# Optimization experiments

Hardware: AMD Instinct MI355X
Metric: run time of the kernel (lower is better)

## Reference

```python
import jax, jax.numpy as jnp
import numpy as np

B, S, D, H, P, K = 2, 1025, 1024, 16, 1024, 32
HD = D // H
G = int(np.sqrt(P))
TEMP = 0.1
CANTOR_W = 0.3
SCALE = HD ** -0.5
EPS_LN = 1e-5


def _layernorm(x, w, b):
    m = jnp.mean(x, axis=-1, keepdims=True)
    v = jnp.mean((x - m) ** 2, axis=-1, keepdims=True)
    return (x - m) * jax.lax.rsqrt(v + EPS_LN) * w + b


def _l2norm(x):
    n = jnp.sqrt(jnp.sum(x * x, axis=-1, keepdims=True))
    return x / jnp.maximum(n, 1e-12)


def _cantor_bias():
    idx = np.arange(P)
    xg, yg = idx % G, idx // G
    s = xg + yg
    z = (s * (s + 1) // 2 + yg).astype(np.float32)
    fp = z / max(z.max(), 1.0)
    dist = np.abs(fp[None, :] - fp[:, None])
    aff = 1.0 - dist
    np.fill_diagonal(aff, -1e9)
    return jnp.asarray(aff * CANTOR_W, dtype=jnp.float32)


def setup_inputs() -> dict:
    key = jax.random.key(0)
    ks = jax.random.split(key, 16)
    std = 0.02
    def w(k, *shape):
        return jax.random.normal(k, shape, dtype=jnp.float32) * std
    inp = {
        'x': jax.random.normal(ks[0], (B, S, D), dtype=jnp.float32),
        'norm1_w': jnp.ones((D,), jnp.float32), 'norm1_b': jnp.zeros((D,), jnp.float32),
        'rq_w': w(ks[1], D, D), 'rq_b': jnp.zeros((D,), jnp.float32),
        'rk_w': w(ks[2], D, D), 'rk_b': jnp.zeros((D,), jnp.float32),
        'pos_bias': _cantor_bias(),
        'qkv_w': w(ks[3], 3 * D, D), 'qkv_b': jnp.zeros((3 * D,), jnp.float32),
        'proj_w': w(ks[4], D, D), 'proj_b': jnp.zeros((D,), jnp.float32),
        'norm2_w': jnp.ones((D,), jnp.float32), 'norm2_b': jnp.zeros((D,), jnp.float32),
        'fc1_w': w(ks[5], 4 * D, D), 'fc1_b': jnp.zeros((4 * D,), jnp.float32),
        'fc2_w': w(ks[6], D, 4 * D), 'fc2_b': jnp.zeros((D,), jnp.float32),
    }
    return inp


def reference(x, norm1_w, norm1_b, rq_w, rq_b, rk_w, rk_b, pos_bias,
              qkv_w, qkv_b, proj_w, proj_b, norm2_w, norm2_b,
              fc1_w, fc1_b, fc2_w, fc2_b):
    x_norm = _layernorm(x, norm1_w, norm1_b)
    # ---- router: content-based top-k wormhole routes over patches ----
    xp = x_norm[:, 1:, :]                                   # [B,P,D]
    q_r = _l2norm(xp @ rq_w.T + rq_b)
    k_r = _l2norm(xp @ rk_w.T + rk_b)
    scores = jnp.einsum('bpd,bqd->bpq', q_r, k_r) + pos_bias[None]
    eye = jnp.eye(P, dtype=bool)
    scores = jnp.where(eye[None], -1e9, scores)
    topk_scores, routes = jax.lax.top_k(scores / TEMP, K)   # [B,P,K]
    route_w = jax.nn.softmax(topk_scores, axis=-1)          # [B,P,K]
    # ---- qkv ----
    qkv = (x_norm @ qkv_w.T + qkv_b).reshape(B, S, 3, H, HD)
    qkv = jnp.transpose(qkv, (2, 0, 3, 1, 4))               # [3,B,H,S,hd]
    Q, Kf, V = qkv[0], qkv[1], qkv[2]
    # CLS token: dense attention over all positions
    Qc = Q[:, :, :1, :]
    attn_cls = jax.nn.softmax(jnp.einsum('bhqd,bhkd->bhqk', Qc, Kf) * SCALE, axis=-1)
    out_cls = jnp.einsum('bhqk,bhkd->bhqd', attn_cls, V)    # [B,H,1,hd]
    # Patches: sparse gather attention via wormhole routes
    Qp, Kp, Vp = Q[:, :, 1:], Kf[:, :, 1:], V[:, :, 1:]     # [B,H,P,hd]
    gather = jax.vmap(lambda t, r: t[:, r])                 # t:[H,P,hd], r:[P,K] -> [H,P,K,hd]
    Kg = gather(Kp, routes)                                  # [B,H,P,K,hd]
    Vg = gather(Vp, routes)
    sp = jnp.einsum('bhpd,bhpkd->bhpk', Qp, Kg) * SCALE
    sp = sp + jnp.clip(jnp.log(route_w), -10.0, None)[:, None]
    attn_p = jax.nn.softmax(sp, axis=-1)
    out_p = jnp.einsum('bhpk,bhpkd->bhpd', attn_p, Vg)      # [B,H,P,hd]
    out = jnp.concatenate([out_cls, out_p], axis=2)          # [B,H,S,hd]
    out = jnp.transpose(out, (0, 2, 1, 3)).reshape(B, S, D)
    x = x + (out @ proj_w.T + proj_b)
    h = _layernorm(x, norm2_w, norm2_b)
    h = jax.nn.gelu(h @ fc1_w.T + fc1_b, approximate=False)
    x = x + (h @ fc2_w.T + fc2_b)
    return x
```

## Files before the change

kernel.cpp:

```cpp
#include <hip/hip_runtime.h>
#include <hip/hip_bf16.h>
#include <math.h>

typedef unsigned short u16;
typedef __attribute__((ext_vector_type(8))) short short8;
typedef __attribute__((ext_vector_type(4))) float f32x4;

#define B_ 2
#define S_ 1025
#define D_ 1024
#define H_ 16
#define HD_ 64
#define P_ 1024
#define K_ 32
#define NS_ 16

static constexpr float TEMP_ = 0.1f;
static constexpr float SCALE_ = 0.125f;
static constexpr float EPS_LN_ = 1e-5f;

__device__ __forceinline__ float bf2f(u16 u) {
  unsigned int t = ((unsigned int)u) << 16;
  float f;
  __builtin_memcpy(&f, &t, 4);
  return f;
}
__device__ __forceinline__ u16 f2bf(float f) {
  __hip_bfloat16 h = __float2bfloat16(f);
  u16 u;
  __builtin_memcpy(&u, &h, 2);
  return u;
}
__device__ __forceinline__ float gelu_f(float x) {
  return 0.5f * x * (1.0f + erff(x * 0.70710678118654752f));
}

typedef __attribute__((address_space(1))) const unsigned int gas_u32;
typedef __attribute__((address_space(3))) unsigned int las_u32;
__device__ __forceinline__ void g2l16(const void* g, void* l) {
  __builtin_amdgcn_global_load_lds((gas_u32*)g, (las_u32*)l, 16, 0, 0);
}

__global__ __launch_bounds__(256) void conv4_kernel(
    const float* __restrict__ s0, int n0, const float* __restrict__ s1, int n1,
    const float* __restrict__ s2, int n2, const float* __restrict__ s3, int n3,
    u16* __restrict__ dst) {
  const int e = (blockIdx.x * 256 + threadIdx.x) * 4;
  const float* src;
  int off;
  if (e < n0) { src = s0; off = e; }
  else if (e < n0 + n1) { src = s1; off = e - n0; }
  else if (e < n0 + n1 + n2) { src = s2; off = e - n0 - n1; }
  else if (e < n0 + n1 + n2 + n3) { src = s3; off = e - n0 - n1 - n2; }
  else return;
  float4 t = *reinterpret_cast<const float4*>(src + off);
  ushort4 o;
  o.x = f2bf(t.x); o.y = f2bf(t.y); o.z = f2bf(t.z); o.w = f2bf(t.w);
  *reinterpret_cast<ushort4*>(dst + e) = o;
}

__device__ __forceinline__ float block_sum256(float v, float* red4) {
  for (int off = 32; off > 0; off >>= 1) v += __shfl_down(v, off);
  if ((threadIdx.x & 63) == 0) red4[threadIdx.x >> 6] = v;
  __syncthreads();
  float r = red4[0] + red4[1] + red4[2] + red4[3];
  __syncthreads();
  return r;
}
__device__ __forceinline__ float block_max256(float v, float* red4) {
  for (int off = 32; off > 0; off >>= 1) v = fmaxf(v, __shfl_down(v, off));
  if ((threadIdx.x & 63) == 0) red4[threadIdx.x >> 6] = v;
  __syncthreads();
  float r = fmaxf(fmaxf(red4[0], red4[1]), fmaxf(red4[2], red4[3]));
  __syncthreads();
  return r;
}

__global__ __launch_bounds__(256) void ln_kernel(const float* __restrict__ x,
                                                 const float* __restrict__ w,
                                                 const float* __restrict__ b,
                                                 u16* __restrict__ out) {
  __shared__ float red4[4];
  const long long base = (long long)blockIdx.x * D_;
  float v[4];
  float s = 0.f, ss = 0.f;
#pragma unroll
  for (int u = 0; u < 4; ++u) {
    int d = threadIdx.x + u * 256;
    float f = x[base + d];
    v[u] = f; s += f; ss += f * f;
  }
  float tot = block_sum256(s, red4);
  float tot2 = block_sum256(ss, red4);
  float mean = tot * (1.0f / D_);
  float var = tot2 * (1.0f / D_) - mean * mean;
  float rstd = rsqrtf(var + EPS_LN_);
#pragma unroll
  for (int u = 0; u < 4; ++u) {
    int d = threadIdx.x + u * 256;
    out[base + d] = f2bf((v[u] - mean) * rstd * w[d] + b[d]);
  }
}

__global__ __launch_bounds__(256) void ln2res_kernel(
    const float* __restrict__ x, const float* __restrict__ pb,
    const float* __restrict__ p0, const float* __restrict__ p1,
    const float* __restrict__ w, const float* __restrict__ b,
    float* __restrict__ x1, u16* __restrict__ out) {
  __shared__ float red4[4];
  const long long base = (long long)blockIdx.x * D_;
  float v[4];
  float s = 0.f, ss = 0.f;
#pragma unroll
  for (int u = 0; u < 4; ++u) {
    int d = threadIdx.x + u * 256;
    float f = x[base + d] + pb[d] + p0[base + d] + p1[base + d];
    x1[base + d] = f;
    v[u] = f; s += f; ss += f * f;
  }
  float tot = block_sum256(s, red4);
  float tot2 = block_sum256(ss, red4);
  float mean = tot * (1.0f / D_);
  float var = tot2 * (1.0f / D_) - mean * mean;
  float rstd = rsqrtf(var + EPS_LN_);
#pragma unroll
  for (int u = 0; u < 4; ++u) {
    int d = threadIdx.x + u * 256;
    out[base + d] = f2bf((v[u] - mean) * rstd * w[d] + b[d]);
  }
}

__global__ __launch_bounds__(256) void fc2red_kernel(
    const float* __restrict__ x1, const float* __restrict__ b,
    const float* __restrict__ p0, const float* __restrict__ p1,
    float* __restrict__ out) {
  const long long base = (long long)blockIdx.x * D_;
#pragma unroll
  for (int u = 0; u < 4; ++u) {
    int d = threadIdx.x + u * 256;
    out[base + d] = x1[base + d] + b[d] + p0[base + d] + p1[base + d];
  }
}

__global__ __launch_bounds__(256) void l2norm2_kernel(u16* __restrict__ qr,
                                                      u16* __restrict__ kr) {
  __shared__ float red4[4];
  const int row = blockIdx.x;
  u16* x = (row < 2048) ? qr + (long long)row * D_
                        : kr + (long long)(row - 2048) * D_;
  float v[4];
  float ss = 0.f;
#pragma unroll
  for (int u = 0; u < 4; ++u) {
    int d = threadIdx.x + u * 256;
    v[u] = bf2f(x[d]);
    ss += v[u] * v[u];
  }
  float tot = block_sum256(ss, red4);
  float inv = 1.0f / fmaxf(sqrtf(tot), 1e-12f);
#pragma unroll
  for (int u = 0; u < 4; ++u) {
    int d = threadIdx.x + u * 256;
    x[d] = f2bf(v[u] * inv);
  }
}

template <int MODE>
__device__ __forceinline__ void gemm_body(
    u16* sA, u16* sW,
    const u16* __restrict__ A, long long a_off, const u16* __restrict__ W,
    int N, int M, int Kd, int klen, int rpb, long long a_bs, long long w_bs,
    const float* __restrict__ bias, const float* __restrict__ bias2, int bias_off,
    u16* __restrict__ outU, u16* __restrict__ outU2, float* __restrict__ outF,
    int bx, int by, int bz) {
  const int tid = threadIdx.x;
  const int lane = tid & 63;
  const int q4 = lane >> 4;
  const int r16 = lane & 15;
  const int wave = tid >> 6;
  const int wr = (wave & 1) * 32;
  const int wc = (wave >> 1) * 64;
  const int row0 = by * 64;
  const int col0 = bx * 128;
  const int batch = row0 / rpb;
  const u16* Ab = A + a_off + (long long)batch * a_bs +
                  (long long)(row0 - batch * rpb) * Kd;
  const u16* Wb = W + (long long)batch * w_bs + (long long)col0 * Kd;
  const int rmax = N - 1 - row0;
  const int srow = tid >> 3;
  const int kx = ((tid & 7) ^ (srow & 7)) * 8;
  const int kbeg = bz * klen;
  const int niter = klen >> 6;
  f32x4 acc[2][4] = {};
  for (int it = 0; it < niter; ++it) {
    const int k0 = kbeg + it * 64;
#pragma unroll
    for (int c = 0; c < 2; ++c) {
      const int rg = c * 32 + srow;
      g2l16(Ab + (long long)min(rg, rmax) * Kd + kx + k0, &sA[c * 2048 + tid * 8]);
    }
#pragma unroll
    for (int c = 0; c < 4; ++c) {
      const int rg = c * 32 + srow;
      g2l16(Wb + (long long)rg * Kd + kx + k0, &sW[c * 2048 + tid * 8]);
    }
    __builtin_amdgcn_s_waitcnt(0);
    __syncthreads();
#pragma unroll
    for (int s = 0; s < 2; ++s) {
      short8 a[2], b[4];
      const int ks = ((s * 4 + q4) ^ (r16 & 7)) * 8;
#pragma unroll
      for (int i = 0; i < 2; ++i)
        a[i] = *reinterpret_cast<const short8*>(&sA[(wr + i * 16 + r16) * 64 + ks]);
#pragma unroll
      for (int j = 0; j < 4; ++j)
        b[j] = *reinterpret_cast<const short8*>(&sW[(wc + j * 16 + r16) * 64 + ks]);
#pragma unroll
      for (int i = 0; i < 2; ++i)
#pragma unroll
        for (int j = 0; j < 4; ++j)
          acc[i][j] = __builtin_amdgcn_mfma_f32_16x16x32_bf16(a[i], b[j],
                                                              acc[i][j], 0, 0, 0);
    }
    __syncthreads();
  }
  const long long sbase = (MODE == 6) ? (long long)bz * bias_off : 0;
#pragma unroll
  for (int i = 0; i < 2; ++i) {
#pragma unroll
    for (int reg = 0; reg < 4; ++reg) {
      const int n = row0 + wr + i * 16 + q4 * 4 + reg;
      if (n >= N) continue;
      const long long nrow = (long long)n * M;
#pragma unroll
      for (int j = 0; j < 4; ++j) {
        const int m = col0 + wc + j * 16 + r16;
        float v = acc[i][j][reg];
        if (MODE == 0) {
          if (m < 1024) outU[(long long)n * 1024 + m] = f2bf(v + bias[m]);
          else outU2[(long long)n * 1024 + m - 1024] = f2bf(v + bias2[m - 1024]);
        } else if (MODE == 2) {
          outU[nrow + m] = f2bf(v + bias[bias_off + m]);
        } else if (MODE == 3) {
          outU[nrow + m] = f2bf(gelu_f(v + bias[bias_off + m]));
        } else {
          outF[sbase + nrow + m] = v;
        }
      }
    }
  }
}

__device__ __forceinline__ int xcd_swz(int orig, int nwg) {
  return (orig & 7) * (nwg >> 3) + (orig >> 3);
}

template <int MODE>
__global__ __launch_bounds__(256, 6) void mfma_gemm(
    const u16* __restrict__ A, long long a_off, const u16* __restrict__ W,
    int N, int M, int Kd, int klen, int rpb, long long a_bs, long long w_bs,
    const float* __restrict__ bias, const float* __restrict__ bias2, int bias_off,
    u16* __restrict__ outU, u16* __restrict__ outU2, float* __restrict__ outF) {
  __shared__ u16 sA[64 * 64];
  __shared__ u16 sW[128 * 64];
  const int gx = gridDim.x, gy = gridDim.y;
  const int nwg = gx * gy * gridDim.z;
  const int orig = blockIdx.x + gx * (blockIdx.y + gy * blockIdx.z);
  const int swz = xcd_swz(orig, nwg);
  const int bx = swz % gx;
  const int t = swz / gx;
  const int by = t % gy;
  const int bz = t / gy;
  gemm_body<MODE>(sA, sW, A, a_off, W, N, M, Kd, klen, rpb, a_bs, w_bs,
                  bias, bias2, bias_off, outU, outU2, outF, bx, by, bz);
}

__global__ __launch_bounds__(256, 6) void fused_rqk_qkv(
    const u16* __restrict__ xnorm, const u16* __restrict__ wslot,
    const float* __restrict__ rq_b, const float* __restrict__ rk_b,
    const float* __restrict__ qkv_b,
    u16* __restrict__ qr, u16* __restrict__ kr, u16* __restrict__ qkvb) {
  __shared__ u16 sA[64 * 64];
  __shared__ u16 sW[128 * 64];
  const int id = xcd_swz(blockIdx.x, 1304);
  if (id < 512) {
    gemm_body<0>(sA, sW, xnorm, 1024LL, wslot,
                 2048, 2048, 1024, 1024, 1024, (long long)S_ * D_, 0LL,
                 rq_b, rk_b, 0, qr, kr, nullptr, id & 15, id >> 4, 0);
  } else {
    const int id2 = id - 512;
    gemm_body<2>(sA, sW, xnorm, 0LL, wslot + (2 << 20),
                 2050, 3072, 1024, 1024, 2050, 0LL, 0LL,
                 qkv_b, nullptr, 0, qkvb, nullptr, nullptr, id2 % 24, id2 / 24, 0);
  }
}

__global__ __launch_bounds__(256) void topk_kernel(const float* __restrict__ s0,
                                                   const float* __restrict__ s1,
                                                   const float* __restrict__ pos,
                                                   int* __restrict__ routes,
                                                   float* __restrict__ logw) {
  const int row = blockIdx.x * 4 + (threadIdx.x >> 6);
  const int lane = threadIdx.x & 63;
  const int p = row & (P_ - 1);
  const float* r0 = s0 + (long long)row * P_;
  const float* r1 = s1 + (long long)row * P_;
  const float* pr = pos + (long long)p * P_;
  float v[16];
#pragma unroll
  for (int j = 0; j < 16; ++j) {
    const int q = j * 64 + lane;
    float t = r0[q] + r1[q] + pr[q];
    v[j] = (q == p) ? -1e9f : t;
  }
  float selv = 0.f;
  int seli = 0;
  for (int t = 0; t < K_; ++t) {
    float bv = v[0];
    int bj = 0;
#pragma unroll
    for (int j = 1; j < 16; ++j)
      if (v[j] > bv) { bv = v[j]; bj = j; }
    int bi = bj * 64 + lane;
#pragma unroll
    for (int off = 1; off < 64; off <<= 1) {
      float ov = __shfl_xor(bv, off);
      int oi = __shfl_xor(bi, off);
      if (ov > bv || (ov == bv && oi < bi)) { bv = ov; bi = oi; }
    }
    if (lane == t) { selv = bv; seli = bi; }
    if ((bi & 63) == lane) v[bi >> 6] = -3.0e38f;
  }
  const float sc = selv * (1.0f / TEMP_);
  const float mt = __shfl(sc, 0);
  float e = (lane < K_) ? expf(sc - mt) : 0.f;
  float sum = e;
#pragma unroll
  for (int off = 1; off < 64; off <<= 1) sum += __shfl_xor(sum, off);
  if (lane < K_) {
    const float lw = sc - mt - logf(sum);
    logw[(long long)row * K_ + lane] = fmaxf(lw, -10.0f);
    routes[(long long)row * K_ + lane] = seli;
  }
}

__global__ __launch_bounds__(256) void attn_cls_p1(const u16* __restrict__ qkv,
                                                   float* __restrict__ part) {
  __shared__ float qs[HD_];
  __shared__ float lg[65];
  __shared__ float red4[4];
  __shared__ float sacc[4][HD_];
  const int ck = blockIdx.x;
  const int bh = blockIdx.y;
  const int b = bh >> 4, h = bh & 15;
  const int tid = threadIdx.x;
  const int lane = tid & 63;
  const int wv = tid >> 6;
  const int s0 = ck * 65;
  const int rows = min(65, S_ - s0);
  const long long base = (long long)b * S_ * 3072;
  if (tid < HD_) qs[tid] = bf2f(qkv[base + h * HD_ + tid]);
  __syncthreads();
  float lmax = -3.0e38f;
  if (tid < rows) {
    const u16* kp = qkv + base + (long long)(s0 + tid) * 3072 + 1024 + h * HD_;
    float d = 0.f;
#pragma unroll
    for (int c = 0; c < 8; ++c) {
      short8 kv = *reinterpret_cast<const short8*>(kp + c * 8);
#pragma unroll
      for (int e = 0; e < 8; ++e) d += qs[c * 8 + e] * bf2f((u16)kv[e]);
    }
    d *= SCALE_;
    lg[tid] = d;
    lmax = d;
  }
  const float m = block_max256(lmax, red4);
  float e = 0.f;
  if (tid < rows) {
    e = expf(lg[tid] - m);
    lg[tid] = e;
  }
  const float l = block_sum256(e, red4);
  __syncthreads();
  float acc = 0.f;
  for (int r = wv; r < rows; r += 4)
    acc += lg[r] * bf2f(qkv[base + (long long)(s0 + r) * 3072 + 2048 + h * HD_ + lane]);
  sacc[wv][lane] = acc;
  __syncthreads();
  float* pc = part + ((long long)bh * NS_ + ck) * 66;
  if (tid < HD_)
    pc[tid] = sacc[0][tid] + sacc[1][tid] + sacc[2][tid] + sacc[3][tid];
  if (tid == 64) pc[64] = m;
  if (tid == 65) pc[65] = l;
}

__global__ __launch_bounds__(64) void attn_cls_p2(const float* __restrict__ part,
                                                  u16* __restrict__ out) {
  const int bh = blockIdx.x;
  const int b = bh >> 4, h = bh & 15;
  const int tid = threadIdx.x;
  const float* pb = part + (long long)bh * NS_ * 66;
  float M = -3.0e38f;
#pragma unroll
  for (int c = 0; c < NS_; ++c) M = fmaxf(M, pb[c * 66 + 64]);
  float L = 0.f, a = 0.f;
#pragma unroll
  for (int c = 0; c < NS_; ++c) {
    const float w = expf(pb[c * 66 + 64] - M);
    L += pb[c * 66 + 65] * w;
    a += pb[c * 66 + tid] * w;
  }
  out[(long long)b * S_ * D_ + h * HD_ + tid] = f2bf(a / L);
}

__global__ __launch_bounds__(64) void attn_patch_kernel(const u16* __restrict__ qkv,
                                                        const int* __restrict__ routes,
                                                        const float* __restrict__ logw,
                                                        u16* __restrict__ out) {
  __shared__ float qs[HD_];
  __shared__ float wk[K_];
  __shared__ int sidx[K_];
  const int bid = blockIdx.x;
  const int h = bid & 15;
  const int p = (bid >> 4) & (P_ - 1);
  const int b = bid >> 14;
  const int tid = threadIdx.x;
  const long long base = (long long)b * S_ * 3072;
  qs[tid] = bf2f(qkv[base + (long long)(1 + p) * 3072 + h * HD_ + tid]);
  __syncthreads();
  float lg = -3.0e38f;
  if (tid < K_) {
    const long long ro = ((long long)(b * P_ + p)) * K_ + tid;
    const int r = routes[ro];
    sidx[tid] = r;
    const u16* kp = qkv + base + (long long)(1 + r) * 3072 + 1024 + h * HD_;
    float d = 0.f;
#pragma unroll
    for (int c = 0; c < 8; ++c) {
      short8 kv = *reinterpret_cast<const short8*>(kp + c * 8);
#pragma unroll
      for (int e = 0; e < 8; ++e) d += qs[c * 8 + e] * bf2f((u16)kv[e]);
    }
    lg = d * SCALE_ + logw[ro];
  }
  float m = lg;
#pragma unroll
  for (int off = 1; off < 32; off <<= 1) m = fmaxf(m, __shfl_xor(m, off));
  float e = (tid < K_) ? expf(lg - m) : 0.f;
  float sum = e;
#pragma unroll
  for (int off = 1; off < 32; off <<= 1) sum += __shfl_xor(sum, off);
  if (tid < K_) wk[tid] = e / sum;
  __syncthreads();
  float acc = 0.f;
#pragma unroll 4
  for (int k = 0; k < K_; ++k)
    acc += wk[k] * bf2f(qkv[base + (long long)(1 + sidx[k]) * 3072 + 2048 + h * HD_ + tid]);
  out[((long long)b * S_ + 1 + p) * D_ + h * HD_ + tid] = f2bf(acc);
}

extern "C" void kernel_launch(void* const* d_in, const int* in_sizes, int n_in,
                              void* d_out, int out_size, void* d_ws, size_t ws_size,
                              hipStream_t stream) {
  const float* x      = (const float*)d_in[0];
  const float* n1w    = (const float*)d_in[1];
  const float* n1b    = (const float*)d_in[2];
  const float* rq_w   = (const float*)d_in[3];
  const float* rq_b   = (const float*)d_in[4];
  const float* rk_w   = (const float*)d_in[5];
  const float* rk_b   = (const float*)d_in[6];
  const float* pos    = (const float*)d_in[7];
  const float* qkv_w  = (const float*)d_in[8];
  const float* qkv_b  = (const float*)d_in[9];
  const float* proj_w = (const float*)d_in[10];
  const float* proj_b = (const float*)d_in[11];
  const float* n2w    = (const float*)d_in[12];
  const float* n2b    = (const float*)d_in[13];
  const float* fc1_w  = (const float*)d_in[14];
  const float* fc1_b  = (const float*)d_in[15];
  const float* fc2_w  = (const float*)d_in[16];
  const float* fc2_b  = (const float*)d_in[17];
  float* out = (float*)d_out;

  char* mem = (char*)d_ws;
  int*   routes = (int*)mem;
  float* logw   = (float*)(mem + 262144);
  float* part   = (float*)(mem + 524288);
  u16*   wslot  = (u16*)(mem + 786432);
  u16*   xnorm  = (u16*)(mem + 17563648);
  u16*   qr     = (u16*)(mem + 21762048);
  u16*   attn   = qr;
  u16*   qkvb   = (u16*)(mem + 25960448);
  u16*   kr     = (u16*)(mem + 38555648);
  u16*   hbuf   = qkvb;
  float* x1     = (float*)(mem + 42758144);
  float* sc_p0 = (float*)(mem + 786432);
  float* sc_p1 = (float*)(mem + 42758144);
  float* pr_p0 = (float*)(mem + 25960448);
  float* pr_p1 = (float*)(mem + 34357248);
  float* fc_p0 = (float*)(mem + 0);
  float* fc_p1 = (float*)(mem + 17563648);

  ln_kernel<<<B_ * S_, 256, 0, stream>>>(x, n1w, n1b, xnorm);

  conv4_kernel<<<6144, 256, 0, stream>>>(rq_w, 1 << 20, rk_w, 1 << 20,
                                         qkv_w, 3 << 20, proj_w, 1 << 20, wslot);

  fused_rqk_qkv<<<1304, 256, 0, stream>>>(xnorm, wslot, rq_b, rk_b, qkv_b,
                                          qr, kr, qkvb);

  l2norm2_kernel<<<4096, 256, 0, stream>>>(qr, kr);

  mfma_gemm<6><<<dim3(8, 32, 2), 256, 0, stream>>>(qr, 0LL, kr,
      2048, 1024, 1024, 512, 1024, 1LL << 20, 1LL << 20,
      nullptr, nullptr, 10492928, nullptr, nullptr, sc_p0);

  topk_kernel<<<512, 256, 0, stream>>>(sc_p0, sc_p1, pos, routes, logw);

  attn_cls_p1<<<dim3(NS_, B_ * H_), 256, 0, stream>>>(qkvb, part);
  attn_cls_p2<<<B_ * H_, 64, 0, stream>>>(part, attn);
  attn_patch_kernel<<<B_ * P_ * H_, 64, 0, stream>>>(qkvb, routes, logw, attn);

  mfma_gemm<6><<<dim3(8, 33, 2), 256, 0, stream>>>(attn, 0LL, wslot + (5 << 20),
      2050, 1024, 1024, 512, 2050, 0LL, 0LL,
      nullptr, nullptr, 2099200, nullptr, nullptr, pr_p0);

  conv4_kernel<<<8192, 256, 0, stream>>>(fc1_w, 1 << 22, fc2_w, 1 << 22,
                                         nullptr, 0, nullptr, 0, wslot);

  ln2res_kernel<<<B_ * S_, 256, 0, stream>>>(x, proj_b, pr_p0, pr_p1,
                                             n2w, n2b, x1, xnorm);

  mfma_gemm<3><<<dim3(32, 33), 256, 0, stream>>>(xnorm, 0LL, wslot,
      2050, 4096, 1024, 1024, 2050, 0LL, 0LL,
      fc1_b, nullptr, 0, hbuf, nullptr, nullptr);
  mfma_gemm<6><<<dim3(8, 33, 2), 256, 0, stream>>>(hbuf, 0LL, wslot + (1 << 22),
      2050, 1024, 4096, 2048, 2050, 0LL, 0LL,
      nullptr, nullptr, 4390912, nullptr, nullptr, fc_p0);
  fc2red_kernel<<<B_ * S_, 256, 0, stream>>>(x1, fc2_b, fc_p0, fc_p1, out);
}
```

Before: 380.0 us.

## Double-buffer LDS tiles in MFMA GEMM to overlap global loads with compute

The shared GEMM body now keeps two LDS buffers for the A and W tiles. It issues the async global-to-LDS copy of the next K-slice before running the MFMAs on the current slice, which is meant to hide global load latency behind matrix math. LDS per block doubles to 48 KB, so the launch bounds drop from 6 to 3 blocks per CU. The explicit s_waitcnt(0) before the barrier is removed, so correctness depends on __syncthreads waiting for the outstanding LDS-DMA loads.

```diff
diff --git a/kernel.cpp b/kernel.cpp
--- a/kernel.cpp
+++ b/kernel.cpp
@@ -192,8 +192,8 @@
   const int kbeg = bz * klen;
   const int niter = klen >> 6;
   f32x4 acc[2][4] = {};
-  for (int it = 0; it < niter; ++it) {
-    const int k0 = kbeg + it * 64;
+  {
+    const int k0 = kbeg;
 #pragma unroll
     for (int c = 0; c < 2; ++c) {
       const int rg = c * 32 + srow;
@@ -204,18 +204,40 @@
       const int rg = c * 32 + srow;
       g2l16(Wb + (long long)rg * Kd + kx + k0, &sW[c * 2048 + tid * 8]);
     }
-    __builtin_amdgcn_s_waitcnt(0);
-    __syncthreads();
+  }
+  __syncthreads();
+  int cur = 0;
+  for (int it = 0; it < niter; ++it) {
+    if (it + 1 < niter) {
+      const int k0 = kbeg + (it + 1) * 64;
+      const int na = (cur ^ 1) * 4096;
+      const int nw = (cur ^ 1) * 8192;
+#pragma unroll
+      for (int c = 0; c < 2; ++c) {
+        const int rg = c * 32 + srow;
+        g2l16(Ab + (long long)min(rg, rmax) * Kd + kx + k0,
+              &sA[na + c * 2048 + tid * 8]);
+      }
+#pragma unroll
+      for (int c = 0; c < 4; ++c) {
+        const int rg = c * 32 + srow;
+        g2l16(Wb + (long long)rg * Kd + kx + k0, &sW[nw + c * 2048 + tid * 8]);
+      }
+    }
+    const int ca = cur * 4096;
+    const int cw = cur * 8192;
 #pragma unroll
     for (int s = 0; s < 2; ++s) {
       short8 a[2], b[4];
       const int ks = ((s * 4 + q4) ^ (r16 & 7)) * 8;
 #pragma unroll
       for (int i = 0; i < 2; ++i)
-        a[i] = *reinterpret_cast<const short8*>(&sA[(wr + i * 16 + r16) * 64 + ks]);
+        a[i] = *reinterpret_cast<const short8*>(
+            &sA[ca + (wr + i * 16 + r16) * 64 + ks]);
 #pragma unroll
       for (int j = 0; j < 4; ++j)
-        b[j] = *reinterpret_cast<const short8*>(&sW[(wc + j * 16 + r16) * 64 + ks]);
+        b[j] = *reinterpret_cast<const short8*>(
+            &sW[cw + (wc + j * 16 + r16) * 64 + ks]);
 #pragma unroll
       for (int i = 0; i < 2; ++i)
 #pragma unroll
@@ -224,6 +246,7 @@
                                                               acc[i][j], 0, 0, 0);
     }
     __syncthreads();
+    cur ^= 1;
   }
   const long long sbase = (MODE == 6) ? (long long)bz * bias_off : 0;
 #pragma unroll
@@ -257,13 +280,13 @@
 }
 
 template <int MODE>
-__global__ __launch_bounds__(256, 6) void mfma_gemm(
+__global__ __launch_bounds__(256, 3) void mfma_gemm(
     const u16* __restrict__ A, long long a_off, const u16* __restrict__ W,
     int N, int M, int Kd, int klen, int rpb, long long a_bs, long long w_bs,
     const float* __restrict__ bias, const float* __restrict__ bias2, int bias_off,
     u16* __restrict__ outU, u16* __restrict__ outU2, float* __restrict__ outF) {
-  __shared__ u16 sA[64 * 64];
-  __shared__ u16 sW[128 * 64];
+  __shared__ u16 sA[2 * 64 * 64];
+  __shared__ u16 sW[2 * 128 * 64];
   const int gx = gridDim.x, gy = gridDim.y;
   const int nwg = gx * gy * gridDim.z;
   const int orig = blockIdx.x + gx * (blockIdx.y + gy * blockIdx.z);
@@ -276,13 +299,13 @@
                   bias, bias2, bias_off, outU, outU2, outF, bx, by, bz);
 }
 
-__global__ __launch_bounds__(256, 6) void fused_rqk_qkv(
+__global__ __launch_bounds__(256, 3) void fused_rqk_qkv(
     const u16* __restrict__ xnorm, const u16* __restrict__ wslot,
     const float* __restrict__ rq_b, const float* __restrict__ rk_b,
     const float* __restrict__ qkv_b,
     u16* __restrict__ qr, u16* __restrict__ kr, u16* __restrict__ qkvb) {
-  __shared__ u16 sA[64 * 64];
-  __shared__ u16 sW[128 * 64];
+  __shared__ u16 sA[2 * 64 * 64];
+  __shared__ u16 sW[2 * 128 * 64];
   const int id = xcd_swz(blockIdx.x, 1304);
   if (id < 512) {
     gemm_body<0>(sA, sW, xnorm, 1024LL, wslot,
```

Measured after the change: 388.6 us. 2.3% more time.
